# Kernel optimization log

Hardware: AMD Instinct MI355X
Metric: run time of the kernel (lower is better)

## Reference

```python
import jax, jax.numpy as jnp
import numpy as np

N = 20000      # nodes
E = 640000     # edges (~32 neighbors/node)
C = 128        # hidden_channels
H = 8          # heads
D = C // H     # per-head dim
G = 50         # num_gaussians
FIL = 128      # num_filters
L = 3          # num_interactions
CUT = 10.0     # cutoff
NZ = 20        # atom/residue vocab
LOG2 = 0.6931471805599453


def ssp(x):
    # ShiftedSoftplus
    return jax.nn.softplus(x) - LOG2


def setup_inputs() -> dict:
    key = jax.random.key(0)
    ks = jax.random.split(key, 30)
    s = 0.05
    inp = {
        'z': jax.random.randint(ks[0], (N,), 0, NZ),
        'pos': jax.random.normal(ks[1], (N, 3), dtype=jnp.float32) * 10.0,
        'edge_index': jax.random.randint(ks[2], (2, E), 0, N),
        'emb': jax.random.normal(ks[3], (NZ, C), dtype=jnp.float32) * s,
        # per-block edge MLP: Linear(G,FIL) -> ssp -> Linear(FIL,FIL)
        'mlp_w1': jax.random.normal(ks[4], (L, G, FIL), dtype=jnp.float32) * s,
        'mlp_b1': jnp.zeros((L, FIL), dtype=jnp.float32),
        'mlp_w2': jax.random.normal(ks[5], (L, FIL, FIL), dtype=jnp.float32) * s,
        'mlp_b2': jnp.zeros((L, FIL), dtype=jnp.float32),
        # TransformerConv params (heads*D == C)
        'wq': jax.random.normal(ks[6], (L, C, C), dtype=jnp.float32) * s,
        'bq': jnp.zeros((L, C), dtype=jnp.float32),
        'wk': jax.random.normal(ks[7], (L, C, C), dtype=jnp.float32) * s,
        'bk': jnp.zeros((L, C), dtype=jnp.float32),
        'wv': jax.random.normal(ks[8], (L, C, C), dtype=jnp.float32) * s,
        'bv': jnp.zeros((L, C), dtype=jnp.float32),
        'we': jax.random.normal(ks[9], (L, FIL, C), dtype=jnp.float32) * s,
        'be': jnp.zeros((L, C), dtype=jnp.float32),
        'wskip': jax.random.normal(ks[10], (L, C, C), dtype=jnp.float32) * s,
        'bskip': jnp.zeros((L, C), dtype=jnp.float32),
        'wl': jax.random.normal(ks[11], (L, C, C), dtype=jnp.float32) * s,
        'bl': jnp.zeros((L, C), dtype=jnp.float32),
        # output head
        'w_o1': jax.random.normal(ks[12], (C, C // 2), dtype=jnp.float32) * s,
        'b_o1': jnp.zeros((C // 2,), dtype=jnp.float32),
        'w_o2': jax.random.normal(ks[13], (C // 2, 1), dtype=jnp.float32) * s,
        'b_o2': jnp.zeros((1,), dtype=jnp.float32),
    }
    return inp


def reference(z, pos, edge_index, emb, mlp_w1, mlp_b1, mlp_w2, mlp_b2,
              wq, bq, wk, bk, wv, bv, we, be, wskip, bskip, wl, bl,
              w_o1, b_o1, w_o2, b_o2):
    src, dst = edge_index[0], edge_index[1]  # source_to_target flow
    # edge distances + Gaussian smearing  -> edge_attr [E, G]
    d = jnp.sqrt(jnp.sum((pos[dst] - pos[src]) ** 2, axis=-1) + 1e-12)
    offset = jnp.linspace(0.0, CUT, G)
    coeff = -0.5 / (offset[1] - offset[0]) ** 2
    edge_attr = jnp.exp(coeff * (d[:, None] - offset) ** 2)

    h = emb[z]  # [N, C]
    scale = 1.0 / jnp.sqrt(jnp.float32(D))
    for l in range(L):
        # edge filter MLP -> e [E, FIL]
        e = ssp(edge_attr @ mlp_w1[l] + mlp_b1[l]) @ mlp_w2[l] + mlp_b2[l]
        ep = (e @ we[l] + be[l]).reshape(E, H, D)          # edge embedding per head
        q = (h @ wq[l] + bq[l]).reshape(N, H, D)
        k = (h @ wk[l] + bk[l]).reshape(N, H, D)[src] + ep  # [E, H, D]
        v = (h @ wv[l] + bv[l]).reshape(N, H, D)[src] + ep  # [E, H, D]
        logits = jnp.sum(q[dst] * k, axis=-1) * scale       # [E, H]
        m = jax.ops.segment_max(logits, dst, num_segments=N)
        m = jnp.where(jnp.isfinite(m), m, 0.0)
        ex = jnp.exp(logits - m[dst])
        den = jax.ops.segment_sum(ex, dst, num_segments=N)
        alpha = ex / (den[dst] + 1e-16)                     # softmax over incoming edges
        agg = jax.ops.segment_sum(alpha[..., None] * v, dst, num_segments=N)
        out = agg.reshape(N, C) + h @ wskip[l] + bskip[l]   # concat heads + root skip
        out = ssp(out)
        out = out @ wl[l] + bl[l]
        h = h + out                                          # residual across blocks
    o = ssp(h @ w_o1 + b_o1) @ w_o2 + b_o2                   # [N, 1]
    return o
```

## Files before the change

### kernel.cpp

```cpp
#include <hip/hip_runtime.h>

#define NN 20000
#define NE 640000
#define CC 128
#define HH 8
#define GG 50
#define FF 128
#define LL 3
#define NTAB 2048
#define DMAX 12.0f

typedef unsigned short u16;
typedef __attribute__((ext_vector_type(8))) short bf16x8;
typedef __attribute__((ext_vector_type(4))) float f32x4;

__device__ __forceinline__ u16 f2bf(float f) {
    union { float f; unsigned int i; } x; x.f = f;
    unsigned int r = x.i + 0x7fffu + ((x.i >> 16) & 1u);
    return (u16)(r >> 16);
}
__device__ __forceinline__ float sspf(float x) {
    return fmaxf(x, 0.0f) + __logf(1.0f + __expf(-fabsf(x))) - 0.69314718055994531f;
}

__global__ void k_pos4(const float* __restrict__ pos, float4* __restrict__ pos4,
                       int* __restrict__ packed) {
    int n = blockIdx.x * 256 + threadIdx.x;
    if (n < NN) {
        float4 v;
        v.x = pos[n * 3 + 0]; v.y = pos[n * 3 + 1]; v.z = pos[n * 3 + 2]; v.w = 0.0f;
        pos4[n] = v;
        packed[n] = 0;
    }
}

__global__ void k_dist(const int* __restrict__ ei, const float4* __restrict__ pos4,
                       int* __restrict__ packed, int* __restrict__ drec) {
    int base = (blockIdx.x * 256 + threadIdx.x) * 4;
    if (base >= NE) return;
    int aa[4], bb[4], rec[4];
    #pragma unroll
    for (int j = 0; j < 4; ++j) {
        int e = base + j;
        aa[j] = ei[e]; bb[j] = ei[NE + e];
    }
    float4 pa[4], pb[4];
    #pragma unroll
    for (int j = 0; j < 4; ++j) { pa[j] = pos4[aa[j]]; pb[j] = pos4[bb[j]]; }
    #pragma unroll
    for (int j = 0; j < 4; ++j) {
        float dx = pb[j].x - pa[j].x, dy = pb[j].y - pa[j].y, dz = pb[j].z - pa[j].z;
        float d = sqrtf(dx * dx + dy * dy + dz * dz + 1e-12f);
        float tt = d * ((float)NTAB / DMAX);
        bool far = tt >= (float)(NTAB - 1);
        int r = -1;
        if (!far) {
            int i0 = (int)tt;
            int fr = min((int)((tt - (float)i0) * 65536.0f), 65535);
            r = (i0 << 16) | fr;
        }
        rec[j] = r;
        drec[base + j] = r;
        atomicAdd(&packed[bb[j]], far ? 1 : 0x10001);
    }
}

__global__ __launch_bounds__(1024) void k_scan(const int* __restrict__ packed,
                                               int* __restrict__ rowptr,
                                               int* __restrict__ curF) {
    __shared__ int sums[1024];
    const int t = threadIdx.x;
    int local[20];
    int base = t * 20;
    int s = 0;
    #pragma unroll
    for (int i = 0; i < 20; ++i) {
        int idx = base + i;
        int v = (idx < NN) ? (packed[idx] & 0xffff) : 0;
        local[i] = s; s += v;
    }
    sums[t] = s;
    __syncthreads();
    for (int off = 1; off < 1024; off <<= 1) {
        int v = (t >= off) ? sums[t - off] : 0;
        __syncthreads();
        sums[t] += v;
        __syncthreads();
    }
    int excl = (t == 0) ? 0 : sums[t - 1];
    #pragma unroll
    for (int i = 0; i < 20; ++i) {
        int idx = base + i;
        if (idx < NN) { int r = excl + local[i]; rowptr[idx] = r; curF[idx] = r; }
    }
    if (t == 1023) rowptr[NN] = sums[1023];
}

__global__ void k_mid(const int* __restrict__ rowptr, const int* __restrict__ packed,
                      int* __restrict__ rowmid, int* __restrict__ curN) {
    int n = blockIdx.x * 256 + threadIdx.x;
    if (n < NN) {
        int m = rowptr[n + 1] - (((unsigned)packed[n]) >> 16);
        rowmid[n] = m; curN[n] = m;
    }
}

__global__ void k_scatter(const int* __restrict__ ei, const int* __restrict__ drec,
                          int* __restrict__ curF, int* __restrict__ curN,
                          int* __restrict__ srcp, int2* __restrict__ erec) {
    int base = (blockIdx.x * 256 + threadIdx.x) * 4;
    if (base >= NE) return;
    int aa[4], bb[4], rec[4], pp[4];
    #pragma unroll
    for (int j = 0; j < 4; ++j) {
        int e = base + j;
        aa[j] = ei[e]; bb[j] = ei[NE + e]; rec[j] = drec[e];
    }
    #pragma unroll
    for (int j = 0; j < 4; ++j)
        pp[j] = atomicAdd((rec[j] == -1) ? &curF[bb[j]] : &curN[bb[j]], 1);
    #pragma unroll
    for (int j = 0; j < 4; ++j) {
        srcp[pp[j]] = aa[j];
        if (rec[j] != -1) { int2 r; r.x = aa[j]; r.y = rec[j]; erec[pp[j]] = r; }
    }
}

__global__ __launch_bounds__(128) void k_prep23(const float* __restrict__ w2,
                                                const float* __restrict__ we,
                                                float* __restrict__ w23f) {
    int l = blockIdx.x >> 7, k = blockIdx.x & 127;
    int cp = threadIdx.x;
    float s = 0.0f;
    for (int c = 0; c < FF; ++c)
        s = fmaf(w2[((size_t)l * FF + k) * FF + c], we[((size_t)l * FF + c) * CC + cp], s);
    w23f[((size_t)l * FF + k) * CC + cp] = s;
}

__global__ __launch_bounds__(128) void k_prepb(const float* __restrict__ b2,
                                               const float* __restrict__ we,
                                               const float* __restrict__ be,
                                               float* __restrict__ b23g) {
    int l = blockIdx.x;
    int cp = threadIdx.x;
    float s = be[l * CC + cp];
    for (int k = 0; k < FF; ++k)
        s = fmaf(b2[l * FF + k], we[((size_t)l * FF + k) * CC + cp], s);
    b23g[l * CC + cp] = s;
}

__global__ __launch_bounds__(128) void k_prept(const float* __restrict__ w1,
                                               const float* __restrict__ b1,
                                               const float* __restrict__ w23f,
                                               const float* __restrict__ b23g,
                                               float* __restrict__ tab) {
    const int l = blockIdx.x / (NTAB + 1);
    const int i = blockIdx.x % (NTAB + 1);
    const int c = threadIdx.x;
    __shared__ float attr[GG];
    __shared__ float hid[FF];
    const float STEP = 10.0f / 49.0f;
    const float COEF = -0.5f / (STEP * STEP);
    float d = (float)i * (DMAX / (float)NTAB);
    if (c < GG) { float df = d - STEP * (float)c; attr[c] = __expf(COEF * df * df); }
    __syncthreads();
    float s = b1[l * FF + c];
    for (int g = 0; g < GG; ++g)
        s = fmaf(attr[g], w1[((size_t)l * GG + g) * FF + c], s);
    hid[c] = sspf(s);
    __syncthreads();
    float o = b23g[l * CC + c];
    for (int k = 0; k < FF; ++k)
        o = fmaf(hid[k], w23f[((size_t)l * FF + k) * CC + c], o);
    tab[((size_t)l * (NTAB + 1) + i) * CC + c] = o;
}

__global__ void k_packt(const float* __restrict__ tab, uint2* __restrict__ tabq) {
    int idx = blockIdx.x * 256 + threadIdx.x;
    if (idx >= LL * NTAB * 64) return;
    int ln = idx & 63;
    int i = (idx >> 6) % NTAB;
    int l = idx / (NTAB * 64);
    int c0 = ln * 2;
    const float* t0 = &tab[((size_t)l * (NTAB + 1) + i) * CC + c0];
    const float* t1 = t0 + CC;
    const float* ti = &tab[((size_t)l * (NTAB + 1) + NTAB) * CC + c0];
    uint2 o;
    o.x = (unsigned)f2bf(t0[0] - ti[0]) | ((unsigned)f2bf(t0[1] - ti[1]) << 16);
    o.y = (unsigned)f2bf(t1[0] - ti[0]) | ((unsigned)f2bf(t1[1] - ti[1]) << 16);
    tabq[((size_t)l * NTAB + i) * 64 + ln] = o;
}

__global__ __launch_bounds__(128) void k_foldb(const float* __restrict__ bk,
                                               const float* __restrict__ bv,
                                               const float* __restrict__ tab,
                                               float* __restrict__ bkf,
                                               float* __restrict__ bvf) {
    int l = blockIdx.x, c = threadIdx.x;
    float ep = tab[((size_t)l * (NTAB + 1) + NTAB) * CC + c];
    bkf[l * CC + c] = bk[l * CC + c] + ep;
    bvf[l * CC + c] = bv[l * CC + c] + ep;
}

__global__ void k_prepn(const float* __restrict__ wq, const float* __restrict__ wk,
                        const float* __restrict__ wv, const float* __restrict__ wsk,
                        const float* __restrict__ wl, u16* __restrict__ wn) {
    int i = blockIdx.x * 256 + threadIdx.x;
    if (i >= LL * 5 * 128 * 128) return;
    int k = i & 127, c = (i >> 7) & 127;
    int lm = i >> 14; int m = lm % 5, l = lm / 5;
    const float* W = (m == 0) ? wq : (m == 1) ? wk : (m == 2) ? wv : (m == 3) ? wsk : wl;
    wn[i] = f2bf(W[((size_t)l * 128 + k) * 128 + c]);
}

template<int MODE>
__global__ __launch_bounds__(256) void k_node(
    const int* __restrict__ z, const float* __restrict__ emb,
    const float* __restrict__ tbuf,
    const u16* __restrict__ wlT, const float* __restrict__ bl,
    float* __restrict__ h,
    const u16* __restrict__ wq4,
    const float* __restrict__ bq, const float* __restrict__ bk,
    const float* __restrict__ bv, const float* __restrict__ bs,
    float* __restrict__ o_q, unsigned int* __restrict__ kvw,
    float* __restrict__ o_skip, int nrows)
{
    __shared__ __align__(16) short tb[64 * 136];
    __shared__ __align__(16) short hb[64 * 136];
    const int t = threadIdx.x, lane = t & 63, w = t >> 6;
    const int tx = lane & 15, tg = lane >> 4;
    const int n0 = blockIdx.x * 64;
    const f32x4 zf4 = { 0.0f, 0.0f, 0.0f, 0.0f };

    if (MODE == 0) {
        for (int idx = t; idx < 64 * 32; idx += 256) {
            int r = idx >> 5, kq = idx & 31;
            int n = n0 + r;
            float4 hv;
            if (n < nrows) {
                hv = *(const float4*)&emb[(size_t)z[n] * CC + kq * 4];
                *(float4*)&h[(size_t)n * CC + kq * 4] = hv;
            } else { hv.x = hv.y = hv.z = hv.w = 0.0f; }
            uint2 pk = make_uint2((unsigned)f2bf(hv.x) | ((unsigned)f2bf(hv.y) << 16),
                                  (unsigned)f2bf(hv.z) | ((unsigned)f2bf(hv.w) << 16));
            *(uint2*)&hb[r * 136 + kq * 4] = pk;
        }
        __syncthreads();
    } else {
        for (int idx = t; idx < 64 * 32; idx += 256) {
            int r = idx >> 5, kq = idx & 31;
            int n = n0 + r;
            float4 tv;
            if (n < nrows) tv = *(const float4*)&tbuf[(size_t)n * 128 + kq * 4];
            else { tv.x = tv.y = tv.z = tv.w = 0.0f; }
            uint2 pk = make_uint2((unsigned)f2bf(tv.x) | ((unsigned)f2bf(tv.y) << 16),
                                  (unsigned)f2bf(tv.z) | ((unsigned)f2bf(tv.w) << 16));
            *(uint2*)&tb[r * 136 + kq * 4] = pk;
        }
        __syncthreads();
        f32x4 acc[2][4];
        #pragma unroll
        for (int mt = 0; mt < 2; ++mt)
            #pragma unroll
            for (int nt = 0; nt < 4; ++nt) acc[mt][nt] = zf4;
        #pragma unroll
        for (int s = 0; s < 4; ++s) {
            bf16x8 af[2], bfr[4];
            #pragma unroll
            for (int mt = 0; mt < 2; ++mt)
                af[mt] = *(const bf16x8*)&wlT[(size_t)(w * 32 + mt * 16 + tx) * 128 + s * 32 + tg * 8];
            #pragma unroll
            for (int nt = 0; nt < 4; ++nt)
                bfr[nt] = *(const bf16x8*)&tb[(nt * 16 + tx) * 136 + s * 32 + tg * 8];
            #pragma unroll
            for (int mt = 0; mt < 2; ++mt)
                #pragma unroll
                for (int nt = 0; nt < 4; ++nt)
                    acc[mt][nt] = __builtin_amdgcn_mfma_f32_16x16x32_bf16(af[mt], bfr[nt], acc[mt][nt], 0, 0, 0);
        }
        #pragma unroll
        for (int mt = 0; mt < 2; ++mt) {
            int c0 = w * 32 + mt * 16 + tg * 4;
            float4 bb = *(const float4*)&bl[c0];
            #pragma unroll
            for (int nt = 0; nt < 4; ++nt) {
                int n = n0 + nt * 16 + tx;
                if (n < nrows) {
                    float4 hv = *(const float4*)&h[(size_t)n * 128 + c0];
                    hv.x += acc[mt][nt][0] + bb.x; hv.y += acc[mt][nt][1] + bb.y;
                    hv.z += acc[mt][nt][2] + bb.z; hv.w += acc[mt][nt][3] + bb.w;
                    *(float4*)&h[(size_t)n * 128 + c0] = hv;
                    if (MODE == 1) {
                        uint2 pk = make_uint2((unsigned)f2bf(hv.x) | ((unsigned)f2bf(hv.y) << 16),
                                              (unsigned)f2bf(hv.z) | ((unsigned)f2bf(hv.w) << 16));
                        *(uint2*)&hb[(nt * 16 + tx) * 136 + c0] = pk;
                    }
                }
            }
        }
        if (MODE == 1) __syncthreads();
    }

    if (MODE <= 1) {
        #pragma unroll
        for (int m = 0; m < 4; ++m) {
            f32x4 acc[2][4];
            #pragma unroll
            for (int mt = 0; mt < 2; ++mt)
                #pragma unroll
                for (int nt = 0; nt < 4; ++nt) acc[mt][nt] = zf4;
            const u16* Wm = wq4 + (size_t)m * 16384;
            #pragma unroll
            for (int s = 0; s < 4; ++s) {
                bf16x8 af[2], bfr[4];
                #pragma unroll
                for (int mt = 0; mt < 2; ++mt)
                    af[mt] = *(const bf16x8*)&Wm[(size_t)(w * 32 + mt * 16 + tx) * 128 + s * 32 + tg * 8];
                #pragma unroll
                for (int nt = 0; nt < 4; ++nt)
                    bfr[nt] = *(const bf16x8*)&hb[(nt * 16 + tx) * 136 + s * 32 + tg * 8];
                #pragma unroll
                for (int mt = 0; mt < 2; ++mt)
                    #pragma unroll
                    for (int nt = 0; nt < 4; ++nt)
                        acc[mt][nt] = __builtin_amdgcn_mfma_f32_16x16x32_bf16(af[mt], bfr[nt], acc[mt][nt], 0, 0, 0);
            }
            const float* Bm = (m == 0) ? bq : (m == 1) ? bk : (m == 2) ? bv : bs;
            if (m == 0 || m == 3) {
                float* Om = (m == 0) ? o_q : o_skip;
                #pragma unroll
                for (int mt = 0; mt < 2; ++mt) {
                    int c0 = w * 32 + mt * 16 + tg * 4;
                    float4 bb = *(const float4*)&Bm[c0];
                    #pragma unroll
                    for (int nt = 0; nt < 4; ++nt) {
                        int n = n0 + nt * 16 + tx;
                        if (n < nrows) {
                            float4 ov;
                            ov.x = acc[mt][nt][0] + bb.x; ov.y = acc[mt][nt][1] + bb.y;
                            ov.z = acc[mt][nt][2] + bb.z; ov.w = acc[mt][nt][3] + bb.w;
                            *(float4*)&Om[(size_t)n * 128 + c0] = ov;
                        }
                    }
                }
            } else {
                const int off = (m == 1) ? 0 : 1;
                #pragma unroll
                for (int mt = 0; mt < 2; ++mt) {
                    int c0 = w * 32 + mt * 16 + tg * 4;
                    float4 bb = *(const float4*)&Bm[c0];
                    #pragma unroll
                    for (int nt = 0; nt < 4; ++nt) {
                        int n = n0 + nt * 16 + tx;
                        if (n < nrows) {
                            unsigned p01 = (unsigned)f2bf(acc[mt][nt][0] + bb.x)
                                         | ((unsigned)f2bf(acc[mt][nt][1] + bb.y) << 16);
                            unsigned p23 = (unsigned)f2bf(acc[mt][nt][2] + bb.z)
                                         | ((unsigned)f2bf(acc[mt][nt][3] + bb.w) << 16);
                            size_t base = (size_t)n * 128 + c0;
                            kvw[base + off] = p01;
                            kvw[base + 2 + off] = p23;
                        }
                    }
                }
            }
        }
    }
}

__global__ __launch_bounds__(256) void k_agg(
    const int* __restrict__ rowptr, const int* __restrict__ rowmid,
    const int* __restrict__ srcp, const int2* __restrict__ erec,
    const uint2* __restrict__ tabq, const float* __restrict__ qn,
    const unsigned int* __restrict__ kvw, const float* __restrict__ skip,
    float* __restrict__ tout)
{
    int wid0 = (blockIdx.x * 256 + threadIdx.x) >> 6;
    if (wid0 >= NN) return;
    const int wid = __builtin_amdgcn_readfirstlane(wid0);
    const int ln = threadIdx.x & 63;
    const int c0 = ln * 2;
    const float SC = 0.25f * 1.4426950408889634f;
    float2 q2 = *(const float2*)&qn[(size_t)wid * CC + c0];
    q2.x *= SC; q2.y *= SC;
    float nx = 0.0f, ny = 0.0f, den = 0.0f;
    int e = rowptr[wid];
    const int emid = rowmid[wid];
    const int eend = rowptr[wid + 1];
    const float FS = 1.52587890625e-5f;

    auto edgeF = [&](uint2 kv) {
        float kex = __uint_as_float(kv.x << 16);
        float key = __uint_as_float(kv.x & 0xffff0000u);
        float vex = __uint_as_float(kv.y << 16);
        float vey = __uint_as_float(kv.y & 0xffff0000u);
        float p = fmaf(q2.x, kex, q2.y * key);
        p += __shfl_xor(p, 1);
        p += __shfl_xor(p, 2);
        p += __shfl_xor(p, 4);
        float w = exp2f(p);
        nx = fmaf(w, vex, nx);
        ny = fmaf(w, vey, ny);
        den += w;
    };
    auto edgeN = [&](uint2 kv, uint2 tp, float fr) {
        float t0x = __uint_as_float(tp.x << 16);
        float t0y = __uint_as_float(tp.x & 0xffff0000u);
        float t1x = __uint_as_float(tp.y << 16);
        float t1y = __uint_as_float(tp.y & 0xffff0000u);
        float ex = fmaf(fr, t1x - t0x, t0x);
        float ey = fmaf(fr, t1y - t0y, t0y);
        float kex = __uint_as_float(kv.x << 16) + ex;
        float key = __uint_as_float(kv.x & 0xffff0000u) + ey;
        float vex = __uint_as_float(kv.y << 16) + ex;
        float vey = __uint_as_float(kv.y & 0xffff0000u) + ey;
        float p = fmaf(q2.x, kex, q2.y * key);
        p += __shfl_xor(p, 1);
        p += __shfl_xor(p, 2);
        p += __shfl_xor(p, 4);
        float w = exp2f(p);
        nx = fmaf(w, vex, nx);
        ny = fmaf(w, vey, ny);
        den += w;
    };

    for (; e + 8 <= emid; e += 8) {
        int s0 = srcp[e + 0], s1 = srcp[e + 1], s2 = srcp[e + 2], s3 = srcp[e + 3];
        int s4 = srcp[e + 4], s5 = srcp[e + 5], s6 = srcp[e + 6], s7 = srcp[e + 7];
        uint2 kv0 = *(const uint2*)&kvw[(size_t)s0 * 128 + c0];
        uint2 kv1 = *(const uint2*)&kvw[(size_t)s1 * 128 + c0];
        uint2 kv2 = *(const uint2*)&kvw[(size_t)s2 * 128 + c0];
        uint2 kv3 = *(const uint2*)&kvw[(size_t)s3 * 128 + c0];
        uint2 kv4 = *(const uint2*)&kvw[(size_t)s4 * 128 + c0];
        uint2 kv5 = *(const uint2*)&kvw[(size_t)s5 * 128 + c0];
        uint2 kv6 = *(const uint2*)&kvw[(size_t)s6 * 128 + c0];
        uint2 kv7 = *(const uint2*)&kvw[(size_t)s7 * 128 + c0];
        edgeF(kv0); edgeF(kv1); edgeF(kv2); edgeF(kv3);
        edgeF(kv4); edgeF(kv5); edgeF(kv6); edgeF(kv7);
    }
    for (; e < emid; ++e) {
        uint2 kv = *(const uint2*)&kvw[(size_t)srcp[e] * 128 + c0];
        edgeF(kv);
    }
    for (; e + 4 <= eend; e += 4) {
        int2 r0 = erec[e + 0], r1 = erec[e + 1], r2 = erec[e + 2], r3 = erec[e + 3];
        uint2 kv0 = *(const uint2*)&kvw[(size_t)r0.x * 128 + c0];
        uint2 kv1 = *(const uint2*)&kvw[(size_t)r1.x * 128 + c0];
        uint2 kv2 = *(const uint2*)&kvw[(size_t)r2.x * 128 + c0];
        uint2 kv3 = *(const uint2*)&kvw[(size_t)r3.x * 128 + c0];
        uint2 tp0 = tabq[(size_t)(r0.y >> 16) * 64 + ln];
        uint2 tp1 = tabq[(size_t)(r1.y >> 16) * 64 + ln];
        uint2 tp2 = tabq[(size_t)(r2.y >> 16) * 64 + ln];
        uint2 tp3 = tabq[(size_t)(r3.y >> 16) * 64 + ln];
        edgeN(kv0, tp0, (float)(r0.y & 0xffff) * FS);
        edgeN(kv1, tp1, (float)(r1.y & 0xffff) * FS);
        edgeN(kv2, tp2, (float)(r2.y & 0xffff) * FS);
        edgeN(kv3, tp3, (float)(r3.y & 0xffff) * FS);
    }
    for (; e < eend; ++e) {
        int2 r = erec[e];
        uint2 kv = *(const uint2*)&kvw[(size_t)r.x * 128 + c0];
        uint2 tp = tabq[(size_t)(r.y >> 16) * 64 + ln];
        edgeN(kv, tp, (float)(r.y & 0xffff) * FS);
    }

    const float2 sk = *(const float2*)&skip[(size_t)wid * CC + c0];
    float inv = 1.0f / (den + 1e-16f);
    float2 o;
    o.x = sspf(fmaf(nx, inv, sk.x));
    o.y = sspf(fmaf(ny, inv, sk.y));
    *(float2*)&tout[(size_t)wid * CC + c0] = o;
}

__global__ __launch_bounds__(64) void k_head(
    const float* __restrict__ h,
    const float* __restrict__ w1, const float* __restrict__ b1,
    const float* __restrict__ w2, const float* __restrict__ b2,
    float* __restrict__ out)
{
    const int n = blockIdx.x;
    const int j = threadIdx.x;
    float acc = 0.0f;
    for (int k = 0; k < CC; ++k)
        acc = fmaf(h[(size_t)n * CC + k], w1[k * 64 + j], acc);
    float m = sspf(acc + b1[j]);
    float o = m * w2[j];
    #pragma unroll
    for (int msk = 32; msk > 0; msk >>= 1) o += __shfl_xor(o, msk);
    if (j == 0) out[n] = o + b2[0];
}

extern "C" void kernel_launch(void* const* d_in, const int* in_sizes, int n_in,
                              void* d_out, int out_size, void* d_ws, size_t ws_size,
                              hipStream_t stream)
{
    const int*   z   = (const int*)d_in[0];
    const float* pos = (const float*)d_in[1];
    const int*   ei  = (const int*)d_in[2];
    const float* emb = (const float*)d_in[3];
    const float* w1  = (const float*)d_in[4];
    const float* b1  = (const float*)d_in[5];
    const float* w2  = (const float*)d_in[6];
    const float* b2  = (const float*)d_in[7];
    const float* wq  = (const float*)d_in[8];
    const float* bq  = (const float*)d_in[9];
    const float* wk  = (const float*)d_in[10];
    const float* bk  = (const float*)d_in[11];
    const float* wv  = (const float*)d_in[12];
    const float* bv  = (const float*)d_in[13];
    const float* we  = (const float*)d_in[14];
    const float* be  = (const float*)d_in[15];
    const float* wsk = (const float*)d_in[16];
    const float* bsk = (const float*)d_in[17];
    const float* wl  = (const float*)d_in[18];
    const float* bl  = (const float*)d_in[19];
    const float* wo1 = (const float*)d_in[20];
    const float* bo1 = (const float*)d_in[21];
    const float* wo2 = (const float*)d_in[22];
    const float* bo2 = (const float*)d_in[23];

    char* p = (char*)d_ws;
    auto alloc = [&](size_t bytes) -> void* {
        void* r = (void*)p; p += (bytes + 255) & ~(size_t)255; return r;
    };
    float* h    = (float*)alloc((size_t)NN * CC * 4);
    float* q    = (float*)alloc((size_t)NN * CC * 4);
    float* skip = (float*)alloc((size_t)NN * CC * 4);
    float* tbuf = (float*)alloc((size_t)NN * CC * 4);
    unsigned int* kvw = (unsigned int*)alloc((size_t)NN * 128 * 4);
    float4* pos4 = (float4*)alloc((size_t)NN * 16);
    float* w23f = (float*)alloc((size_t)LL * FF * CC * 4);
    float* b23g = (float*)alloc((size_t)LL * CC * 4);
    float* tab  = (float*)alloc((size_t)LL * (NTAB + 1) * CC * 4);
    uint2* tabq = (uint2*)alloc((size_t)LL * NTAB * 64 * 8);
    float* bkf  = (float*)alloc((size_t)LL * CC * 4);
    float* bvf  = (float*)alloc((size_t)LL * CC * 4);
    u16*   wn   = (u16*)alloc((size_t)LL * 5 * 128 * 128 * 2);
    int* packed = (int*)alloc((size_t)NN * 4);
    int* rowptr = (int*)alloc((size_t)(NN + 1) * 4);
    int* rowmid = (int*)alloc((size_t)NN * 4);
    int* curF   = (int*)alloc((size_t)NN * 4);
    int* curN   = (int*)alloc((size_t)NN * 4);
    int* srcp   = (int*)alloc((size_t)NE * 4);
    int* drec   = (int*)alloc((size_t)NE * 4);
    int2* erec  = (int2*)alloc((size_t)NE * 8);

    k_pos4<<<(NN + 255) / 256, 256, 0, stream>>>(pos, pos4, packed);
    k_dist<<<(NE / 4 + 255) / 256, 256, 0, stream>>>(ei, pos4, packed, drec);
    k_scan<<<1, 1024, 0, stream>>>(packed, rowptr, curF);
    k_mid<<<(NN + 255) / 256, 256, 0, stream>>>(rowptr, packed, rowmid, curN);
    k_scatter<<<(NE / 4 + 255) / 256, 256, 0, stream>>>(ei, drec, curF, curN, srcp, erec);
    k_prep23<<<LL * 128, 128, 0, stream>>>(w2, we, w23f);
    k_prepb<<<LL, 128, 0, stream>>>(b2, we, be, b23g);
    k_prept<<<LL * (NTAB + 1), 128, 0, stream>>>(w1, b1, w23f, b23g, tab);
    k_packt<<<(LL * NTAB * 64 + 255) / 256, 256, 0, stream>>>(tab, tabq);
    k_foldb<<<LL, 128, 0, stream>>>(bk, bv, tab, bkf, bvf);
    k_prepn<<<(LL * 5 * 128 * 128 + 255) / 256, 256, 0, stream>>>(wq, wk, wv, wsk, wl, wn);

    const int NT = (NN + 63) / 64;
    k_node<0><<<NT, 256, 0, stream>>>(z, emb, nullptr, nullptr, nullptr, h,
        wn, bq, bkf, bvf, bsk, q, kvw, skip, NN);
    for (int l = 0; l < LL; ++l) {
        k_agg<<<(NN * 64 + 255) / 256, 256, 0, stream>>>(rowptr, rowmid, srcp, erec,
            tabq + (size_t)l * NTAB * 64, q, kvw, skip, tbuf);
        const u16* wnl = wn + (size_t)l * 5 * 16384;
        if (l < LL - 1) {
            const u16* wnn = wn + (size_t)(l + 1) * 5 * 16384;
            k_node<1><<<NT, 256, 0, stream>>>(nullptr, nullptr, tbuf,
                wnl + 4 * 16384, bl + l * CC, h,
                wnn, bq + (l + 1) * CC, bkf + (l + 1) * CC,
                bvf + (l + 1) * CC, bsk + (l + 1) * CC,
                q, kvw, skip, NN);
        } else {
            k_node<2><<<NT, 256, 0, stream>>>(nullptr, nullptr, tbuf,
                wnl + 4 * 16384, bl + l * CC, h,
                nullptr, nullptr, nullptr, nullptr, nullptr,
                nullptr, nullptr, nullptr, NN);
        }
    }
    k_head<<<NN, 64, 0, stream>>>(h, wo1, bo1, wo2, bo2, (float*)d_out);
}
```

Baseline: 382.5 us.

## Fuse output head into final node kernel, store aggregation output as bf16

Moves the output MLP head into the last node kernel as an MFMA on the bf16 h tile, using a pre-transposed bf16 copy of w_o1. This removes the separate per-node k_head launch and its re-read of h, and the final layer no longer writes h. The aggregation kernel now writes its output as packed bf16 instead of fp32, halving that buffer's traffic and dropping a conversion in the node kernel. k_mid is folded into k_scan. The head now runs in bf16 precision instead of fp32, adding rounding error to the output.

```diff
diff --git a/kernel.cpp b/kernel.cpp
--- a/kernel.cpp
+++ b/kernel.cpp
@@ -38,7 +38,7 @@
                        int* __restrict__ packed, int* __restrict__ drec) {
     int base = (blockIdx.x * 256 + threadIdx.x) * 4;
     if (base >= NE) return;
-    int aa[4], bb[4], rec[4];
+    int aa[4], bb[4];
     #pragma unroll
     for (int j = 0; j < 4; ++j) {
         int e = base + j;
@@ -59,7 +59,6 @@
             int fr = min((int)((tt - (float)i0) * 65536.0f), 65535);
             r = (i0 << 16) | fr;
         }
-        rec[j] = r;
         drec[base + j] = r;
         atomicAdd(&packed[bb[j]], far ? 1 : 0x10001);
     }
@@ -67,7 +66,9 @@
 
 __global__ __launch_bounds__(1024) void k_scan(const int* __restrict__ packed,
                                                int* __restrict__ rowptr,
-                                               int* __restrict__ curF) {
+                                               int* __restrict__ curF,
+                                               int* __restrict__ rowmid,
+                                               int* __restrict__ curN) {
     __shared__ int sums[1024];
     const int t = threadIdx.x;
     int local[20];
@@ -91,18 +92,15 @@
     #pragma unroll
     for (int i = 0; i < 20; ++i) {
         int idx = base + i;
-        if (idx < NN) { int r = excl + local[i]; rowptr[idx] = r; curF[idx] = r; }
+        if (idx < NN) {
+            int pk = packed[idx];
+            int r = excl + local[i];
+            rowptr[idx] = r; curF[idx] = r;
+            int m = r + (pk & 0xffff) - (int)(((unsigned)pk) >> 16);
+            rowmid[idx] = m; curN[idx] = m;
+        }
     }
     if (t == 1023) rowptr[NN] = sums[1023];
-}
-
-__global__ void k_mid(const int* __restrict__ rowptr, const int* __restrict__ packed,
-                      int* __restrict__ rowmid, int* __restrict__ curN) {
-    int n = blockIdx.x * 256 + threadIdx.x;
-    if (n < NN) {
-        int m = rowptr[n + 1] - (((unsigned)packed[n]) >> 16);
-        rowmid[n] = m; curN[n] = m;
-    }
 }
 
 __global__ void k_scatter(const int* __restrict__ ei, const int* __restrict__ drec,
@@ -204,26 +202,35 @@
 
 __global__ void k_prepn(const float* __restrict__ wq, const float* __restrict__ wk,
                         const float* __restrict__ wv, const float* __restrict__ wsk,
-                        const float* __restrict__ wl, u16* __restrict__ wn) {
+                        const float* __restrict__ wl, const float* __restrict__ wo1,
+                        u16* __restrict__ wn) {
     int i = blockIdx.x * 256 + threadIdx.x;
-    if (i >= LL * 5 * 128 * 128) return;
-    int k = i & 127, c = (i >> 7) & 127;
-    int lm = i >> 14; int m = lm % 5, l = lm / 5;
-    const float* W = (m == 0) ? wq : (m == 1) ? wk : (m == 2) ? wv : (m == 3) ? wsk : wl;
-    wn[i] = f2bf(W[((size_t)l * 128 + k) * 128 + c]);
+    if (i < LL * 5 * 128 * 128) {
+        int k = i & 127, c = (i >> 7) & 127;
+        int lm = i >> 14; int m = lm % 5, l = lm / 5;
+        const float* W = (m == 0) ? wq : (m == 1) ? wk : (m == 2) ? wv : (m == 3) ? wsk : wl;
+        wn[i] = f2bf(W[((size_t)l * 128 + k) * 128 + c]);
+    } else if (i < LL * 5 * 128 * 128 + 64 * 128) {
+        int j = i - LL * 5 * 128 * 128;
+        int k = j & 127, c = j >> 7;
+        wn[i] = f2bf(wo1[k * 64 + c]);
+    }
 }
 
 template<int MODE>
 __global__ __launch_bounds__(256) void k_node(
     const int* __restrict__ z, const float* __restrict__ emb,
-    const float* __restrict__ tbuf,
+    const unsigned int* __restrict__ tbp,
     const u16* __restrict__ wlT, const float* __restrict__ bl,
     float* __restrict__ h,
     const u16* __restrict__ wq4,
     const float* __restrict__ bq, const float* __restrict__ bk,
     const float* __restrict__ bv, const float* __restrict__ bs,
     float* __restrict__ o_q, unsigned int* __restrict__ kvw,
-    float* __restrict__ o_skip, int nrows)
+    float* __restrict__ o_skip,
+    const u16* __restrict__ wo1T, const float* __restrict__ bo1,
+    const float* __restrict__ wo2, const float* __restrict__ bo2,
+    float* __restrict__ outp, int nrows)
 {
     __shared__ __align__(16) short tb[64 * 136];
     __shared__ __align__(16) short hb[64 * 136];
@@ -250,11 +257,8 @@
         for (int idx = t; idx < 64 * 32; idx += 256) {
             int r = idx >> 5, kq = idx & 31;
             int n = n0 + r;
-            float4 tv;
-            if (n < nrows) tv = *(const float4*)&tbuf[(size_t)n * 128 + kq * 4];
-            else { tv.x = tv.y = tv.z = tv.w = 0.0f; }
-            uint2 pk = make_uint2((unsigned)f2bf(tv.x) | ((unsigned)f2bf(tv.y) << 16),
-                                  (unsigned)f2bf(tv.z) | ((unsigned)f2bf(tv.w) << 16));
+            uint2 pk = make_uint2(0u, 0u);
+            if (n < nrows) pk = *(const uint2*)&tbp[(size_t)n * 64 + kq * 2];
             *(uint2*)&tb[r * 136 + kq * 4] = pk;
         }
         __syncthreads();
@@ -285,20 +289,19 @@
             #pragma unroll
             for (int nt = 0; nt < 4; ++nt) {
                 int n = n0 + nt * 16 + tx;
+                uint2 pk = make_uint2(0u, 0u);
                 if (n < nrows) {
                     float4 hv = *(const float4*)&h[(size_t)n * 128 + c0];
                     hv.x += acc[mt][nt][0] + bb.x; hv.y += acc[mt][nt][1] + bb.y;
                     hv.z += acc[mt][nt][2] + bb.z; hv.w += acc[mt][nt][3] + bb.w;
-                    *(float4*)&h[(size_t)n * 128 + c0] = hv;
-                    if (MODE == 1) {
-                        uint2 pk = make_uint2((unsigned)f2bf(hv.x) | ((unsigned)f2bf(hv.y) << 16),
-                                              (unsigned)f2bf(hv.z) | ((unsigned)f2bf(hv.w) << 16));
-                        *(uint2*)&hb[(nt * 16 + tx) * 136 + c0] = pk;
-                    }
+                    if (MODE == 1) *(float4*)&h[(size_t)n * 128 + c0] = hv;
+                    pk = make_uint2((unsigned)f2bf(hv.x) | ((unsigned)f2bf(hv.y) << 16),
+                                    (unsigned)f2bf(hv.z) | ((unsigned)f2bf(hv.w) << 16));
                 }
+                *(uint2*)&hb[(nt * 16 + tx) * 136 + c0] = pk;
             }
         }
-        if (MODE == 1) __syncthreads();
+        __syncthreads();
     }
 
     if (MODE <= 1) {
@@ -365,6 +368,42 @@
                 }
             }
         }
+    } else {
+        f32x4 acc[4];
+        #pragma unroll
+        for (int nt = 0; nt < 4; ++nt) acc[nt] = zf4;
+        #pragma unroll
+        for (int s = 0; s < 4; ++s) {
+            bf16x8 af = *(const bf16x8*)&wo1T[(size_t)(w * 16 + tx) * 128 + s * 32 + tg * 8];
+            bf16x8 bfr[4];
+            #pragma unroll
+            for (int nt = 0; nt < 4; ++nt)
+                bfr[nt] = *(const bf16x8*)&hb[(nt * 16 + tx) * 136 + s * 32 + tg * 8];
+            #pragma unroll
+            for (int nt = 0; nt < 4; ++nt)
+                acc[nt] = __builtin_amdgcn_mfma_f32_16x16x32_bf16(af, bfr[nt], acc[nt], 0, 0, 0);
+        }
+        __syncthreads();
+        float* hsum = (float*)tb;
+        #pragma unroll
+        for (int nt = 0; nt < 4; ++nt) {
+            int c0 = w * 16 + tg * 4;
+            float4 b1v = *(const float4*)&bo1[c0];
+            float4 w2v = *(const float4*)&wo2[c0];
+            float pl = sspf(acc[nt][0] + b1v.x) * w2v.x
+                     + sspf(acc[nt][1] + b1v.y) * w2v.y
+                     + sspf(acc[nt][2] + b1v.z) * w2v.z
+                     + sspf(acc[nt][3] + b1v.w) * w2v.w;
+            pl += __shfl_xor(pl, 16);
+            pl += __shfl_xor(pl, 32);
+            if (tg == 0) hsum[w * 64 + nt * 16 + tx] = pl;
+        }
+        __syncthreads();
+        if (t < 64) {
+            int n = n0 + t;
+            if (n < nrows)
+                outp[n] = hsum[t] + hsum[64 + t] + hsum[128 + t] + hsum[192 + t] + bo2[0];
+        }
     }
 }
 
@@ -373,7 +412,7 @@
     const int* __restrict__ srcp, const int2* __restrict__ erec,
     const uint2* __restrict__ tabq, const float* __restrict__ qn,
     const unsigned int* __restrict__ kvw, const float* __restrict__ skip,
-    float* __restrict__ tout)
+    unsigned int* __restrict__ tout)
 {
     int wid0 = (blockIdx.x * 256 + threadIdx.x) >> 6;
     if (wid0 >= NN) return;
@@ -466,28 +505,9 @@
 
     const float2 sk = *(const float2*)&skip[(size_t)wid * CC + c0];
     float inv = 1.0f / (den + 1e-16f);
-    float2 o;
-    o.x = sspf(fmaf(nx, inv, sk.x));
-    o.y = sspf(fmaf(ny, inv, sk.y));
-    *(float2*)&tout[(size_t)wid * CC + c0] = o;
-}
-
-__global__ __launch_bounds__(64) void k_head(
-    const float* __restrict__ h,
-    const float* __restrict__ w1, const float* __restrict__ b1,
-    const float* __restrict__ w2, const float* __restrict__ b2,
-    float* __restrict__ out)
-{
-    const int n = blockIdx.x;
-    const int j = threadIdx.x;
-    float acc = 0.0f;
-    for (int k = 0; k < CC; ++k)
-        acc = fmaf(h[(size_t)n * CC + k], w1[k * 64 + j], acc);
-    float m = sspf(acc + b1[j]);
-    float o = m * w2[j];
-    #pragma unroll
-    for (int msk = 32; msk > 0; msk >>= 1) o += __shfl_xor(o, msk);
-    if (j == 0) out[n] = o + b2[0];
+    float ox = sspf(fmaf(nx, inv, sk.x));
+    float oy = sspf(fmaf(ny, inv, sk.y));
+    tout[(size_t)wid * 64 + ln] = (unsigned)f2bf(ox) | ((unsigned)f2bf(oy) << 16);
 }
 
 extern "C" void kernel_launch(void* const* d_in, const int* in_sizes, int n_in,
@@ -526,7 +546,7 @@
     float* h    = (float*)alloc((size_t)NN * CC * 4);
     float* q    = (float*)alloc((size_t)NN * CC * 4);
     float* skip = (float*)alloc((size_t)NN * CC * 4);
-    float* tbuf = (float*)alloc((size_t)NN * CC * 4);
+    unsigned int* tbp = (unsigned int*)alloc((size_t)NN * 64 * 4);
     unsigned int* kvw = (unsigned int*)alloc((size_t)NN * 128 * 4);
     float4* pos4 = (float4*)alloc((size_t)NN * 16);
     float* w23f = (float*)alloc((size_t)LL * FF * CC * 4);
@@ -535,7 +555,7 @@
     uint2* tabq = (uint2*)alloc((size_t)LL * NTAB * 64 * 8);
     float* bkf  = (float*)alloc((size_t)LL * CC * 4);
     float* bvf  = (float*)alloc((size_t)LL * CC * 4);
-    u16*   wn   = (u16*)alloc((size_t)LL * 5 * 128 * 128 * 2);
+    u16*   wn   = (u16*)alloc(((size_t)LL * 5 * 128 * 128 + 64 * 128) * 2);
     int* packed = (int*)alloc((size_t)NN * 4);
     int* rowptr = (int*)alloc((size_t)(NN + 1) * 4);
     int* rowmid = (int*)alloc((size_t)NN * 4);
@@ -547,36 +567,39 @@
 
     k_pos4<<<(NN + 255) / 256, 256, 0, stream>>>(pos, pos4, packed);
     k_dist<<<(NE / 4 + 255) / 256, 256, 0, stream>>>(ei, pos4, packed, drec);
-    k_scan<<<1, 1024, 0, stream>>>(packed, rowptr, curF);
-    k_mid<<<(NN + 255) / 256, 256, 0, stream>>>(rowptr, packed, rowmid, curN);
+    k_scan<<<1, 1024, 0, stream>>>(packed, rowptr, curF, rowmid, curN);
     k_scatter<<<(NE / 4 + 255) / 256, 256, 0, stream>>>(ei, drec, curF, curN, srcp, erec);
     k_prep23<<<LL * 128, 128, 0, stream>>>(w2, we, w23f);
     k_prepb<<<LL, 128, 0, stream>>>(b2, we, be, b23g);
     k_prept<<<LL * (NTAB + 1), 128, 0, stream>>>(w1, b1, w23f, b23g, tab);
     k_packt<<<(LL * NTAB * 64 + 255) / 256, 256, 0, stream>>>(tab, tabq);
     k_foldb<<<LL, 128, 0, stream>>>(bk, bv, tab, bkf, bvf);
-    k_prepn<<<(LL * 5 * 128 * 128 + 255) / 256, 256, 0, stream>>>(wq, wk, wv, wsk, wl, wn);
-
+    k_prepn<<<(LL * 5 * 128 * 128 + 64 * 128 + 255) / 256, 256, 0, stream>>>(
+        wq, wk, wv, wsk, wl, wo1, wn);
+
+    const u16* wo1T = wn + (size_t)LL * 5 * 16384;
     const int NT = (NN + 63) / 64;
     k_node<0><<<NT, 256, 0, stream>>>(z, emb, nullptr, nullptr, nullptr, h,
-        wn, bq, bkf, bvf, bsk, q, kvw, skip, NN);
+        wn, bq, bkf, bvf, bsk, q, kvw, skip,
+        nullptr, nullptr, nullptr, nullptr, nullptr, NN);
     for (int l = 0; l < LL; ++l) {
         k_agg<<<(NN * 64 + 255) / 256, 256, 0, stream>>>(rowptr, rowmid, srcp, erec,
-            tabq + (size_t)l * NTAB * 64, q, kvw, skip, tbuf);
+            tabq + (size_t)l * NTAB * 64, q, kvw, skip, tbp);
         const u16* wnl = wn + (size_t)l * 5 * 16384;
         if (l < LL - 1) {
             const u16* wnn = wn + (size_t)(l + 1) * 5 * 16384;
-            k_node<1><<<NT, 256, 0, stream>>>(nullptr, nullptr, tbuf,
+            k_node<1><<<NT, 256, 0, stream>>>(nullptr, nullptr, tbp,
                 wnl + 4 * 16384, bl + l * CC, h,
                 wnn, bq + (l + 1) * CC, bkf + (l + 1) * CC,
                 bvf + (l + 1) * CC, bsk + (l + 1) * CC,
-                q, kvw, skip, NN);
+                q, kvw, skip,
+                nullptr, nullptr, nullptr, nullptr, nullptr, NN);
         } else {
-            k_node<2><<<NT, 256, 0, stream>>>(nullptr, nullptr, tbuf,
+            k_node<2><<<NT, 256, 0, stream>>>(nullptr, nullptr, tbp,
                 wnl + 4 * 16384, bl + l * CC, h,
                 nullptr, nullptr, nullptr, nullptr, nullptr,
-                nullptr, nullptr, nullptr, NN);
-        }
-    }
-    k_head<<<NN, 64, 0, stream>>>(h, wo1, bo1, wo2, bo2, (float*)d_out);
-}
+                nullptr, nullptr, nullptr,
+                wo1T, bo1, wo2, bo2, (float*)d_out, NN);
+        }
+    }
+}
```

New measurement: 398.5 us. 4.2% more time.
